# Performance work log

Hardware: AMD Instinct MI355X
Metric: run time of the kernel (lower is better)

Reference implementation:

```python
import jax, jax.numpy as jnp
import numpy as np

B, N = 128, 256
EPS = float(np.finfo(np.float32).eps)  # torch clamp_probs epsilon for fp32


def to_z(logits, u):
    # torch.distributions.utils.clamp_probs + Gumbel perturbation
    uc = jnp.clip(u, EPS, 1.0 - EPS)
    return logits + (-jnp.log(-jnp.log(uc)))


def _find_cycle(heads):
    # heads[j] = parent of j; node 0 is the root (heads[0] == 0).
    L = len(heads)
    color = np.zeros(L, dtype=np.int8)  # 0 unvisited, 1 on path, 2 done
    color[0] = 2
    for start in range(1, L):
        if color[start]:
            continue
        path = []
        v = start
        while color[v] == 0:
            color[v] = 1
            path.append(v)
            v = int(heads[v])
        if color[v] == 1:  # found a cycle
            i = path.index(v)
            return path[i:]
        for p in path:
            color[p] = 2
    return None


def _chu_liu(score):
    # score[h, d] = weight of edge h -> d; diag and column 0 are -inf.
    L = score.shape[0]
    heads = score.argmax(axis=0)
    heads[0] = 0
    cyc = _find_cycle(heads)
    if cyc is None:
        return heads
    cyc = np.asarray(cyc)
    mask = np.ones(L, dtype=bool)
    mask[cyc] = False
    non = np.where(mask)[0]  # includes root 0
    n = len(non)
    cyc_head_sc = score[heads[cyc], cyc]  # [|C|] chosen in-edge weights of cycle nodes
    # contracted score matrix: nodes = non-cycle nodes + one supernode (index n)
    new = np.full((n + 1, n + 1), -np.inf, dtype=score.dtype)
    new[:n, :n] = score[np.ix_(non, non)]
    into = score[np.ix_(non, cyc)] - cyc_head_sc[None, :]  # gain of entering cycle at each node
    arg_into = into.argmax(axis=1)
    new[:n, n] = into[np.arange(n), arg_into]
    outo = score[np.ix_(cyc, non)]
    arg_out = outo.argmax(axis=0)
    new[n, :n] = outo[arg_out, np.arange(n)]
    nh = _chu_liu(new)
    # expand
    heads_out = np.empty(L, dtype=np.int64)
    nh_non = nh[:n]
    safe = np.clip(nh_non, 0, n - 1)
    heads_out[non] = np.where(nh_non == n, cyc[arg_out], non[safe])
    heads_out[cyc] = heads[cyc]
    hc = int(nh[n])  # head of the contracted supernode (index into non)
    heads_out[cyc[arg_into[hc]]] = non[hc]  # break the cycle at the entry node
    heads_out[0] = 0
    return heads_out


def edmonds_batch(z, lengths):
    # z: np [B, N, N] edge scores z[b, h, d]; root = node 0; per-graph size lengths[b].
    Bn, Nn, _ = z.shape
    arb = np.zeros((Bn, Nn, Nn), dtype=np.float32)
    stats = np.zeros((Bn,), dtype=np.float32)
    for b in range(Bn):  # irregular sequential graph algorithm: per-graph host loop
        L = int(lengths[b])
        s = z[b, :L, :L].astype(np.float64).copy()
        np.fill_diagonal(s, -np.inf)
        s[:, 0] = -np.inf  # no incoming edges to root
        heads = _chu_liu(s)
        deps = np.arange(1, L)
        arb[b, heads[deps], deps] = 1.0
        stats[b] = z[b, heads[deps], deps].sum()
    return jnp.asarray(arb), jnp.asarray(stats)


def setup_inputs():
    key = jax.random.key(0)
    k1, k2, k3 = jax.random.split(key, 3)
    logits = jax.random.normal(k1, (B, N, N), dtype=jnp.float32)
    u = jax.random.uniform(k2, (B, N, N), dtype=jnp.float32)
    lengths = jax.random.randint(k3, (B,), 2, N + 1, dtype=jnp.int32)
    return {"logits": logits, "u": u, "lengths": lengths}


def reference(logits, u, lengths):
    z = to_z(logits, u)  # Gumbel-perturbed scores (differentiable part)
    arb, stats = edmonds_batch(np.asarray(z), np.asarray(lengths))
    return (arb, stats, z)
```

## Files before the change

### kernel.cpp

```cpp
#include <hip/hip_runtime.h>
#include <cmath>

static constexpr int Bn = 128;
static constexpr int Nn = 256;
static constexpr int META_PB = 131072;

template <typename T>
__global__ __launch_bounds__(256) void zinit_kernel(
    const float* __restrict__ logits,
    const float* __restrict__ u,
    float* __restrict__ zout,
    float* __restrict__ arb,
    T* __restrict__ M)
{
    int idx = blockIdx.x * blockDim.x + threadIdx.x;
    int j = idx & (Nn - 1);
    int i = (idx >> 8) & (Nn - 1);
    const float EPS = 1.1920928955078125e-07f;
    float uv = u[idx];
    uv = fminf(fmaxf(uv, EPS), 1.0f - EPS);
    float z = logits[idx] - logf(-logf(uv));
    zout[idx] = z;
    arb[idx] = 0.0f;
    M[idx] = (i == j || j == 0) ? (T)(-INFINITY) : (T)z;
}

__device__ __forceinline__ int sel4(int v, int a0, int a1, int a2, int a3) {
    int x0 = __shfl(a0, v & 63);
    int x1 = __shfl(a1, v & 63);
    int x2 = __shfl(a2, v & 63);
    int x3 = __shfl(a3, v & 63);
    int s = v >> 6;
    return s == 0 ? x0 : (s == 1 ? x1 : (s == 2 ? x2 : x3));
}

template <typename T>
__global__ __launch_bounds__(256) void edmonds_kernel(
    const int* __restrict__ lengths,
    const float* __restrict__ zout,
    T* __restrict__ Mg,
    unsigned char* __restrict__ metag,
    float* __restrict__ arb,
    float* __restrict__ stats)
{
    const int b = blockIdx.x;
    const int t = threadIdx.x;
    const int lane = t & 63, wv = t >> 6;
    T* M = Mg + (size_t)b * (Nn * Nn);
    unsigned char* meta = metag + (size_t)b * META_PB;
    const float* zb = zout + (size_t)b * (Nn * Nn);

    __shared__ unsigned short act[256];
    __shared__ unsigned short h[256];
    __shared__ unsigned short h2[256];
    __shared__ unsigned short inv_[256];
    __shared__ unsigned short cyc_c[256];
    __shared__ unsigned short non_c[256];
    __shared__ unsigned short cslot_s[256];
    __shared__ unsigned short resc[256];
    __shared__ unsigned short lev_n[256], lev_c[256];
    __shared__ int lev_off[256];
    __shared__ unsigned char in_cyc[256];
    __shared__ T hval[256];
    __shared__ T chs[256];
    __shared__ double red[256];
    __shared__ int wcnt[4];
    __shared__ int sh_clen, sh_cnt, sh_wslot;

    const int L = lengths[b];

    act[t] = (unsigned short)t;
    in_cyc[t] = 0;
    if (t < L) {
        T best = -INFINITY; int bi = 0;
        const T* col = M + t;
        for (int i = 0; i < L; ++i) {
            T v = col[i * Nn];
            if (v > best) { best = v; bi = i; }
        }
        h[t] = (t == 0) ? (unsigned short)0 : (unsigned short)bi;
        hval[t] = best;
    } else {
        h[t] = 0;
        hval[t] = (T)0;
    }
    __syncthreads();

    int Lc = L, depth = 0, moff = 0;

    while (true) {
        if (wv == 0) {
            int h0 = h[lane], h1 = h[64 | lane], h2r = h[128 | lane], h3 = h[192 | lane];
            int p0 = h0, p1 = h1, p2 = h2r, p3 = h3;
            const int rounds = 32 - __clz(Lc - 1);
            for (int r = 0; r < rounds; ++r) {
                int n0 = sel4(p0, p0, p1, p2, p3);
                int n1 = sel4(p1, p0, p1, p2, p3);
                int n2 = sel4(p2, p0, p1, p2, p3);
                int n3 = sel4(p3, p0, p1, p2, p3);
                p0 = n0; p1 = n1; p2 = n2; p3 = n3;
            }
            unsigned cand = 0xFFFFu;
            if (lane >= 1 && lane < Lc && p0 != 0) cand = (unsigned)lane;
            { int i1 = 64 | lane;  if (i1 < Lc && p1 != 0) cand = min(cand, (unsigned)i1); }
            { int i2 = 128 | lane; if (i2 < Lc && p2 != 0) cand = min(cand, (unsigned)i2); }
            { int i3 = 192 | lane; if (i3 < Lc && p3 != 0) cand = min(cand, (unsigned)i3); }
            for (int m = 1; m < 64; m <<= 1)
                cand = min(cand, (unsigned)__shfl((int)cand, (lane ^ m) & 63));
            if (cand == 0xFFFFu) {
                if (lane == 0) sh_clen = 0;
            } else {
                const int w = sel4((int)cand, p0, p1, p2, p3);
                int cl = 0, v = w;
                do {
                    if (lane == 0) { cyc_c[cl] = (unsigned short)v; in_cyc[v] = 1; }
                    ++cl;
                    v = sel4(v, h0, h1, h2r, h3);
                } while (v != w);
                if (lane == 0) {
                    sh_clen = cl;
                    sh_wslot = act[w];
                    sh_cnt = 0;
                }
            }
        }
        __syncthreads();
        const int clen = sh_clen;
        if (clen == 0) break;
        const int n = Lc - clen;
        const int wslot = sh_wslot;

        const bool fl = (t < Lc) && !in_cyc[t];
        unsigned long long mask = __ballot(fl);
        if (lane == 0) wcnt[wv] = __popcll(mask);
        __syncthreads();

        if (fl) {
            int base = 0;
            for (int k = 0; k < wv; ++k) base += wcnt[k];
            int pos = base + __popcll(mask & ((1ull << lane) - 1ull));
            non_c[pos] = (unsigned short)t;
            inv_[t] = (unsigned short)pos;
        }
        if (t < clen) {
            const int cc = cyc_c[t];
            chs[t] = hval[cc];
            cslot_s[t] = act[cc];
        }
        __syncthreads();

        T vin_r = (T)0, vout_r = (T)0;
        unsigned char argin_r = 0, argout_r = 0;
        int slot_r = 0;
        if (t < n) {
            slot_r = act[non_c[t]];
            T bv = -INFINITY; int bi = 0;
            T bo = -INFINITY; int bj = 0;
            for (int c = 0; c < clen; ++c) {
                const int cs = cslot_s[c];
                T vi = M[slot_r * Nn + cs] - chs[c];
                T vo = M[cs * Nn + slot_r];
                if (vi > bv) { bv = vi; bi = c; }
                if (vo > bo) { bo = vo; bj = c; }
            }
            vin_r = bv; argin_r = (unsigned char)bi;
            vout_r = bo; argout_r = (unsigned char)bj;
        }
        unsigned char* mp = meta + moff;
        if (t < n) {
            mp[t] = (unsigned char)non_c[t];
            mp[n + t] = argin_r;
            mp[2 * n + t] = argout_r;
            M[slot_r * Nn + wslot] = vin_r;
            M[wslot * Nn + slot_r] = vout_r;
        }
        if (t < clen) {
            mp[3 * n + t] = (unsigned char)cyc_c[t];
            mp[3 * n + clen + t] = (unsigned char)h[cyc_c[t]];
        }
        if (t == 0) {
            M[wslot * Nn + wslot] = (T)(-INFINITY);
            lev_n[depth] = (unsigned short)n;
            lev_c[depth] = (unsigned short)clen;
            lev_off[depth] = moff;
        }
        unsigned short myact = 0, myh = 0; T myhval = (T)0; bool need = false;
        if (t < n) {
            const int oc = non_c[t];
            myact = act[oc];
            const int ho = h[oc];
            need = (in_cyc[ho] != 0);
            if (!need) { myh = inv_[ho]; myhval = hval[oc]; }
        }
        __syncthreads();

        if (t < n) {
            act[t] = myact;
            if (!need) { h[t] = myh; hval[t] = myhval; }
            else { int kk = atomicAdd(&sh_cnt, 1); resc[kk] = (unsigned short)t; }
        }
        if (t == 0) {
            act[n] = (unsigned short)wslot;
            int kk = atomicAdd(&sh_cnt, 1); resc[kk] = (unsigned short)n;
            h[0] = 0;
        }
        in_cyc[t] = 0;
        __syncthreads();
        moff += 3 * n + 2 * clen;
        ++depth;
        Lc = n + 1;

        const int nr = sh_cnt;
        if (t < nr) {
            const int jc = resc[t];
            const int cslot = act[jc];
            T best = -INFINITY; int bi = 0;
            for (int i = 0; i < Lc; ++i) {
                T v = M[(int)act[i] * Nn + cslot];
                if (v > best) { best = v; bi = i; }
            }
            h[jc] = (unsigned short)bi;
            hval[jc] = best;
        }
        __syncthreads();
    }

    unsigned short* hcur = h;
    unsigned short* hnew = h2;
    for (int lvl = depth - 1; lvl >= 0; --lvl) {
        const int n = lev_n[lvl];
        const int c = lev_c[lvl];
        const unsigned char* mp = meta + lev_off[lvl];
        const unsigned char* pnon    = mp;
        const unsigned char* pargin  = mp + n;
        const unsigned char* pargout = mp + 2 * n;
        const unsigned char* pcyc    = mp + 3 * n;
        const unsigned char* phcyc   = mp + 3 * n + c;
        if (t < n) {
            const int x = hcur[t];
            hnew[pnon[t]] = (x == n) ? (unsigned short)pcyc[pargout[t]]
                                     : (unsigned short)pnon[x];
        }
        if (t < c) hnew[pcyc[t]] = phcyc[t];
        __syncthreads();
        if (t == 0) {
            const int hc = hcur[n];
            hnew[pcyc[pargin[hc]]] = pnon[hc];
            hnew[0] = 0;
        }
        __syncthreads();
        unsigned short* tmp = hcur; hcur = hnew; hnew = tmp;
    }

    double acc = 0.0;
    if (t >= 1 && t < L) {
        const int hd = hcur[t];
        arb[(size_t)b * (Nn * Nn) + hd * Nn + t] = 1.0f;
        acc = (double)zb[hd * Nn + t];
    }
    red[t] = acc;
    __syncthreads();
    for (int s = 128; s > 0; s >>= 1) {
        if (t < s) red[t] += red[t + s];
        __syncthreads();
    }
    if (t == 0) stats[b] = (float)red[0];
}

extern "C" void kernel_launch(void* const* d_in, const int* in_sizes, int n_in,
                              void* d_out, int out_size, void* d_ws, size_t ws_size,
                              hipStream_t stream)
{
    const float* logits  = (const float*)d_in[0];
    const float* u       = (const float*)d_in[1];
    const int*   lengths = (const int*)d_in[2];

    float* out   = (float*)d_out;
    float* arb   = out;
    float* stats = out + (size_t)Bn * Nn * Nn;
    float* zout  = stats + Bn;

    const int total = Bn * Nn * Nn;
    const int zblocks = total / 256;

    const size_t needD = (size_t)Bn * Nn * Nn * sizeof(double) + (size_t)Bn * META_PB;

    if (ws_size >= needD) {
        double* M = (double*)d_ws;
        unsigned char* meta = (unsigned char*)d_ws + (size_t)Bn * Nn * Nn * sizeof(double);
        zinit_kernel<double><<<zblocks, 256, 0, stream>>>(logits, u, zout, arb, M);
        edmonds_kernel<double><<<Bn, 256, 0, stream>>>(lengths, zout, M, meta, arb, stats);
    } else {
        float* M = (float*)d_ws;
        unsigned char* meta = (unsigned char*)d_ws + (size_t)Bn * Nn * Nn * sizeof(float);
        zinit_kernel<float><<<zblocks, 256, 0, stream>>>(logits, u, zout, arb, M);
        edmonds_kernel<float><<<Bn, 256, 0, stream>>>(lengths, zout, M, meta, arb, stats);
    }
}
```

Before: 855.1 us.

## Use LDS pointer jumping for cycle detection and wave-parallel column argmax recompute

Cycle detection now does pointer jumping through shared-memory arrays instead of cross-lane shuffles with four-way select, and the cycle walk runs on a single lane reading h directly. The per-round recompute of best incoming edges for affected nodes now gives each column to a whole wavefront, with strided loads and a shuffle argmax reduction, instead of one thread scanning the whole column serially. This targets the serial, latency-bound column scans and the shuffle-heavy jumping loop, at the cost of LDS traffic and wave-level reductions.

```diff
diff --git a/kernel.cpp b/kernel.cpp
--- a/kernel.cpp
+++ b/kernel.cpp
@@ -25,15 +25,6 @@
     M[idx] = (i == j || j == 0) ? (T)(-INFINITY) : (T)z;
 }
 
-__device__ __forceinline__ int sel4(int v, int a0, int a1, int a2, int a3) {
-    int x0 = __shfl(a0, v & 63);
-    int x1 = __shfl(a1, v & 63);
-    int x2 = __shfl(a2, v & 63);
-    int x3 = __shfl(a3, v & 63);
-    int s = v >> 6;
-    return s == 0 ? x0 : (s == 1 ? x1 : (s == 2 ? x2 : x3));
-}
-
 template <typename T>
 __global__ __launch_bounds__(256) void edmonds_kernel(
     const int* __restrict__ lengths,
@@ -53,6 +44,8 @@
     __shared__ unsigned short act[256];
     __shared__ unsigned short h[256];
     __shared__ unsigned short h2[256];
+    __shared__ unsigned short p1[256];
+    __shared__ unsigned short p2[256];
     __shared__ unsigned short inv_[256];
     __shared__ unsigned short cyc_c[256];
     __shared__ unsigned short non_c[256];
@@ -90,38 +83,37 @@
 
     while (true) {
         if (wv == 0) {
-            int h0 = h[lane], h1 = h[64 | lane], h2r = h[128 | lane], h3 = h[192 | lane];
-            int p0 = h0, p1 = h1, p2 = h2r, p3 = h3;
+            volatile unsigned short* pa = p1;
+            volatile unsigned short* pb = p2;
+            for (int s = 0; s < 4; ++s) {
+                const int i = (s << 6) | lane;
+                if (i < Lc) pa[i] = h[i];
+            }
             const int rounds = 32 - __clz(Lc - 1);
             for (int r = 0; r < rounds; ++r) {
-                int n0 = sel4(p0, p0, p1, p2, p3);
-                int n1 = sel4(p1, p0, p1, p2, p3);
-                int n2 = sel4(p2, p0, p1, p2, p3);
-                int n3 = sel4(p3, p0, p1, p2, p3);
-                p0 = n0; p1 = n1; p2 = n2; p3 = n3;
+                for (int s = 0; s < 4; ++s) {
+                    const int i = (s << 6) | lane;
+                    if (i < Lc) pb[i] = pa[pa[i]];
+                }
+                volatile unsigned short* tmp = pa; pa = pb; pb = tmp;
             }
             unsigned cand = 0xFFFFu;
-            if (lane >= 1 && lane < Lc && p0 != 0) cand = (unsigned)lane;
-            { int i1 = 64 | lane;  if (i1 < Lc && p1 != 0) cand = min(cand, (unsigned)i1); }
-            { int i2 = 128 | lane; if (i2 < Lc && p2 != 0) cand = min(cand, (unsigned)i2); }
-            { int i3 = 192 | lane; if (i3 < Lc && p3 != 0) cand = min(cand, (unsigned)i3); }
+            for (int s = 0; s < 4; ++s) {
+                const int i = (s << 6) | lane;
+                if (i >= 1 && i < Lc && pa[i] != 0) { cand = min(cand, (unsigned)i); break; }
+            }
             for (int m = 1; m < 64; m <<= 1)
                 cand = min(cand, (unsigned)__shfl((int)cand, (lane ^ m) & 63));
             if (cand == 0xFFFFu) {
                 if (lane == 0) sh_clen = 0;
-            } else {
-                const int w = sel4((int)cand, p0, p1, p2, p3);
+            } else if (lane == 0) {
+                int w = pa[cand];
                 int cl = 0, v = w;
-                do {
-                    if (lane == 0) { cyc_c[cl] = (unsigned short)v; in_cyc[v] = 1; }
-                    ++cl;
-                    v = sel4(v, h0, h1, h2r, h3);
-                } while (v != w);
-                if (lane == 0) {
-                    sh_clen = cl;
-                    sh_wslot = act[w];
-                    sh_cnt = 0;
-                }
+                do { cyc_c[cl++] = (unsigned short)v; in_cyc[v] = 1; v = h[v]; }
+                while (v != w);
+                sh_clen = cl;
+                sh_wslot = act[w];
+                sh_cnt = 0;
             }
         }
         __syncthreads();
@@ -211,16 +203,20 @@
         Lc = n + 1;
 
         const int nr = sh_cnt;
-        if (t < nr) {
-            const int jc = resc[t];
+        for (int r0 = wv; r0 < nr; r0 += 4) {
+            const int jc = resc[r0];
             const int cslot = act[jc];
             T best = -INFINITY; int bi = 0;
-            for (int i = 0; i < Lc; ++i) {
+            for (int i = lane; i < Lc; i += 64) {
                 T v = M[(int)act[i] * Nn + cslot];
                 if (v > best) { best = v; bi = i; }
             }
-            h[jc] = (unsigned short)bi;
-            hval[jc] = best;
+            for (int m = 1; m < 64; m <<= 1) {
+                T ob = __shfl_xor(best, m);
+                int oi = __shfl_xor(bi, m);
+                if (ob > best || (ob == best && oi < bi)) { best = ob; bi = oi; }
+            }
+            if (lane == 0) { h[jc] = (unsigned short)bi; hval[jc] = best; }
         }
         __syncthreads();
     }
```

After: 1.696 ms. 98.3% more time.
